# Performance work log

Measured on AMD Instinct MI355X. Metric: run time of the kernel, lower is better.

Reference implementation:

```python
import jax, jax.numpy as jnp
import numpy as np
import math

NHID = 32
FEAT_SIZE = 32
FEAT_SIZE_LIST = [16, 32, 32, 32]
SEQ_LEN = len(FEAT_SIZE_LIST)   # 4
N_EDGE_LABELS = 3
NLAYERS = 2
N_GRAPHS = 64
FINAL = SEQ_LEN * NHID          # 128


def _pos_enc(max_len, dim):
    pe = np.zeros((max_len, dim), dtype=np.float32)
    pos = np.arange(max_len, dtype=np.float32)[:, None]
    div = np.exp(np.arange(0, dim, 2, dtype=np.float32) * (-math.log(10000.0) / dim))
    pe[:, 0::2] = np.sin(pos * div)
    pe[:, 1::2] = np.cos(pos * div)
    return jnp.asarray(pe)


def _feature_attention(x, wqkv, w1, b1, w2, b2):
    # x: [N, S*NHID] -> attention over the S feature 'tokens' per node
    N, D = x.shape
    S = D // NHID
    xr = x.reshape(N, S, NHID)
    qkv = jnp.einsum('nsf,fh->nsh', xr, wqkv)          # [N,S,3*NHID]
    q, k, v = jnp.split(qkv, 3, axis=-1)
    att = jax.nn.softmax(jnp.einsum('nsh,nth->nst', q, k) / jnp.sqrt(jnp.asarray(NHID, x.dtype)), axis=-1)
    y = jnp.einsum('nst,nth->nsh', att, v)             # [N,S,NHID]
    y = y + (jax.nn.relu(y @ w1 + b1) @ w2 + b2)       # residual FFN
    return y.reshape(N, -1)


def setup_inputs() -> dict:
    key = jax.random.key(0)
    ks = jax.random.split(key, 16)
    N = 100000
    E = 800000
    inp = {
        'x': jax.random.normal(ks[0], (N, 112), dtype=jnp.float32),
        'edge_index0': jax.random.randint(ks[1], (2, E), 0, N),
        'edge_index1': jax.random.randint(ks[2], (2, E), 0, N),
        'edge_index2': jax.random.randint(ks[3], (2, E), 0, N),
        'batch': jnp.sort(jax.random.randint(ks[4], (N,), 0, N_GRAPHS)),
    }
    s = 0.05
    # FeatureLinear encoder (bias-free)
    inp['W_emb'] = jax.random.normal(ks[5], (FEAT_SIZE, NHID), dtype=jnp.float32) * s
    # Per layer: [root, conv0, conv1, conv2] FeatureAttention params, stacked
    A = 1 + N_EDGE_LABELS
    inp['qkv'] = jax.random.normal(ks[6], (NLAYERS, A, NHID, 3 * NHID), dtype=jnp.float32) * s
    inp['ffn_w1'] = jax.random.normal(ks[7], (NLAYERS, A, NHID, NHID), dtype=jnp.float32) * s
    inp['ffn_b1'] = jnp.zeros((NLAYERS, A, NHID), dtype=jnp.float32)
    inp['ffn_w2'] = jax.random.normal(ks[8], (NLAYERS, A, NHID, NHID), dtype=jnp.float32) * s
    inp['ffn_b2'] = jnp.zeros((NLAYERS, A, NHID), dtype=jnp.float32)
    # Heuristic decoder MLP: 128 -> 128 -> 1
    inp['mlp_w1'] = jax.random.normal(ks[9], (FINAL, FINAL), dtype=jnp.float32) * s
    inp['mlp_b1'] = jnp.zeros((FINAL,), dtype=jnp.float32)
    inp['mlp_w2'] = jax.random.normal(ks[10], (FINAL, 1), dtype=jnp.float32) * s
    inp['mlp_b2'] = jnp.zeros((1,), dtype=jnp.float32)
    return inp


def reference(x, edge_index0, edge_index1, edge_index2, batch,
              W_emb, qkv, ffn_w1, ffn_b1, ffn_w2, ffn_b2,
              mlp_w1, mlp_b1, mlp_w2, mlp_b2):
    N = x.shape[0]
    edge_indices = [edge_index0, edge_index1, edge_index2]

    # padding: split by feat_size_list, right-pad each chunk to FEAT_SIZE
    offs = np.cumsum(FEAT_SIZE_LIST)[:-1].tolist()
    chunks = jnp.split(x, offs, axis=1)
    padded = [jnp.pad(c, ((0, 0), (0, FEAT_SIZE - c.shape[1]))) for c in chunks]
    h = jnp.concatenate(padded, axis=1)                       # [N, SEQ_LEN*FEAT_SIZE]

    # sinusoidal positional encoding over the SEQ_LEN feature tokens
    pe = _pos_enc(10, FEAT_SIZE)[:SEQ_LEN]                    # [SEQ_LEN, FEAT_SIZE]
    h = (h.reshape(N, SEQ_LEN, FEAT_SIZE) + pe[None]).reshape(N, -1)

    # FeatureLinear encoder: per-token linear FEAT_SIZE -> NHID
    h = jnp.einsum('nsf,fh->nsh', h.reshape(N, SEQ_LEN, FEAT_SIZE), W_emb).reshape(N, -1)

    # RGNN layers: root attention + per-edge-label attention->scatter-sum
    for l in range(NLAYERS):
        x_out = _feature_attention(h, qkv[l, 0], ffn_w1[l, 0], ffn_b1[l, 0], ffn_w2[l, 0], ffn_b2[l, 0])
        for e in range(N_EDGE_LABELS):
            a = e + 1
            xt = _feature_attention(h, qkv[l, a], ffn_w1[l, a], ffn_b1[l, a], ffn_w2[l, a], ffn_b2[l, a])
            src, dst = edge_indices[e][0], edge_indices[e][1]
            x_out = x_out + jax.ops.segment_sum(xt[src], dst, num_segments=N)
        h = jax.nn.relu(x_out)

    # global mean pool over graphs
    sums = jax.ops.segment_sum(h, batch, num_segments=N_GRAPHS)
    cnts = jax.ops.segment_sum(jnp.ones((N,), h.dtype), batch, num_segments=N_GRAPHS)
    g = sums / jnp.maximum(cnts, 1.0)[:, None]                # [G, FINAL]

    # heuristic decoder
    out = jax.nn.relu(g @ mlp_w1 + mlp_b1) @ mlp_w2 + mlp_b2  # [G, 1]
    return out.squeeze(1)                                     # [G]
```

## Files before the change

### kernel.cpp

```cpp
#include <hip/hip_runtime.h>
#include <hip/hip_bf16.h>
#include <cstdint>
#include <cstddef>


typedef __attribute__((ext_vector_type(8))) short bf16x8;
typedef __attribute__((ext_vector_type(4))) float f32x4;
typedef __attribute__((ext_vector_type(2))) float f32x2;

#if defined(__has_builtin)
#if __has_builtin(__builtin_amdgcn_cvt_pk_fp8_f32) && __has_builtin(__builtin_amdgcn_cvt_pk_f32_fp8)
#define HW_FP8 1
#endif
#if __has_builtin(__builtin_amdgcn_cvt_pk_bf16_f32)
#define HW_PKBF16 1
#endif
#endif

__device__ inline short f2bf(float f) {
    union { float f; unsigned u; } v; v.f = f;
    unsigned r = (v.u + 0x7FFFu + ((v.u >> 16) & 1u)) >> 16;
    return (short)r;
}
__device__ inline float bf2f(unsigned short b) {
    union { unsigned u; float f; } v; v.u = ((unsigned)b) << 16;
    return v.f;
}
#ifdef HW_PKBF16
typedef __attribute__((ext_vector_type(2))) __bf16 bf16x2_t;
__device__ inline unsigned pk2(float a, float b) {
    union { bf16x2_t v; unsigned u; } c;
    c.v = __builtin_amdgcn_cvt_pk_bf16_f32(a, b);
    return c.u;
}
#else
__device__ inline unsigned pk2(float a, float b) {
    unsigned ua = __float_as_uint(a) + 0x8000u;
    unsigned ub = __float_as_uint(b) + 0x8000u;
    return __builtin_amdgcn_perm(ub, ua, 0x07060302u);
}
#endif

#ifndef HW_FP8
__device__ inline unsigned char f2fp8_sw(float f) {
    unsigned s = (__float_as_uint(f) >> 31) & 1u;
    float a = fminf(fabsf(f), 448.f);
    unsigned char bits;
    if (a < 0.015625f) {
        bits = (unsigned char)__float2int_rn(a * 512.f);
    } else {
        int e; float m = frexpf(a, &e);
        int mf = __float2int_rn(m * 16.f);
        if (mf == 16) { mf = 8; e += 1; }
        int ef = e - 1 + 7;
        if (ef > 15) { ef = 15; mf = 14; }
        bits = (unsigned char)((ef << 3) | (mf & 7));
    }
    return (unsigned char)((s << 7) | bits);
}
__device__ inline float fp82f_sw(unsigned b) {
    int s = (b >> 7) & 1, e = (b >> 3) & 15, m = b & 7;
    float v = e ? ldexpf((float)(8 + m), e - 10) : ldexpf((float)m, -9);
    return s ? -v : v;
}
#endif

__device__ inline unsigned pk4fp8(float v0, float v1, float v2, float v3) {
#ifdef HW_FP8
    int w = __builtin_amdgcn_cvt_pk_fp8_f32(v0, v1, 0, false);
    w = __builtin_amdgcn_cvt_pk_fp8_f32(v2, v3, w, true);
    return (unsigned)w;
#else
    return (unsigned)f2fp8_sw(v0) | ((unsigned)f2fp8_sw(v1) << 8) |
           ((unsigned)f2fp8_sw(v2) << 16) | ((unsigned)f2fp8_sw(v3) << 24);
#endif
}
__device__ inline float2 up2fp8(unsigned short raw) {
#ifdef HW_FP8
    f32x2 f = __builtin_amdgcn_cvt_pk_f32_fp8((int)(unsigned)raw, false);
    return make_float2(f[0], f[1]);
#else
    return make_float2(fp82f_sw(raw & 0xffu), fp82f_sw((raw >> 8) & 0xffu));
#endif
}

__device__ inline void acc8(float* a, uint2 v) {
#ifdef HW_FP8
    f32x2 f0 = __builtin_amdgcn_cvt_pk_f32_fp8((int)v.x, false);
    f32x2 f1 = __builtin_amdgcn_cvt_pk_f32_fp8((int)v.x, true);
    f32x2 f2 = __builtin_amdgcn_cvt_pk_f32_fp8((int)v.y, false);
    f32x2 f3 = __builtin_amdgcn_cvt_pk_f32_fp8((int)v.y, true);
    a[0] += f0[0]; a[1] += f0[1]; a[2] += f1[0]; a[3] += f1[1];
    a[4] += f2[0]; a[5] += f2[1]; a[6] += f3[0]; a[7] += f3[1];
#else
    unsigned b0 = v.x, b1 = v.y;
#pragma unroll
    for (int j = 0; j < 4; ++j) a[j]     += fp82f_sw((b0 >> (8 * j)) & 0xffu);
#pragma unroll
    for (int j = 0; j < 4; ++j) a[4 + j] += fp82f_sw((b1 >> (8 * j)) & 0xffu);
#endif
}

__global__ __launch_bounds__(64) void wprep_kernel(
    const float* __restrict__ qkv, const float* __restrict__ fw1,
    const float* __restrict__ fw2, unsigned short* __restrict__ wpack,
    int* __restrict__ bcnt, int* __restrict__ gres,
    float* __restrict__ gsum, float* __restrict__ gcnt)
{
    const int pi = blockIdx.x;
    const int lane = threadIdx.x;
    const int gid = pi * 64 + lane;
    for (int i = gid; i < 256; i += 512) { bcnt[i] = 0; gres[i] = 0; }
    for (int i = gid; i < 64 * 128; i += 512) gsum[i] = 0.f;
    if (gid < 64) gcnt[gid] = 0.f;

    const int q = lane >> 4, m = lane & 15;
    const float* Wq = qkv + (size_t)pi * 32 * 96;
    const float* W1 = fw1 + (size_t)pi * 32 * 32;
    const float* W2 = fw2 + (size_t)pi * 32 * 32;
    unsigned short* dst = wpack + (size_t)pi * 10 * 64 * 8;
#pragma unroll
    for (int ci = 0; ci < 6; ++ci)
#pragma unroll
        for (int j = 0; j < 8; ++j)
            dst[(ci * 64 + lane) * 8 + j] =
                (unsigned short)f2bf(Wq[(q * 8 + j) * 96 + ci * 16 + m]);
#pragma unroll
    for (int t = 0; t < 2; ++t)
#pragma unroll
        for (int j = 0; j < 8; ++j) {
            dst[((6 + t) * 64 + lane) * 8 + j] =
                (unsigned short)f2bf(W1[(q * 8 + j) * 32 + t * 16 + m]);
            dst[((8 + t) * 64 + lane) * 8 + j] =
                (unsigned short)f2bf(W2[(q * 8 + j) * 32 + t * 16 + m]);
        }
}

__global__ __launch_bounds__(128) void enc_kernel(
    const float* __restrict__ x, const float* __restrict__ Wemb,
    unsigned short* __restrict__ h, int N)
{
    __shared__ float sxr[8 * 112];
    __shared__ float spe[128];
    __shared__ float sW[1024];
    const int t = threadIdx.x;
    const int n0 = blockIdx.x * 8;

    {
        int s = t >> 5, f = t & 31;
        int i2 = f >> 1;
        float div = __expf(-(float)(2 * i2) * (logf(10000.0f) / 32.0f));
        float ang = (float)s * div;
        spe[t] = (f & 1) ? cosf(ang) : sinf(ang);
    }
    for (int i = t; i < 1024; i += 128) sW[i] = Wemb[i];
    for (int i = t; i < 8 * 112; i += 128) {
        int n = n0 + i / 112;
        sxr[i] = (n < N) ? x[(size_t)n0 * 112 + i] : 0.f;
    }
    __syncthreads();

    const int ts = t >> 5, c = t & 31;
    const int offs_[4] = {0, 16, 48, 80};
    const int lens_[4] = {16, 32, 32, 32};
    const int off = offs_[ts], len = lens_[ts];

    float acc[8];
#pragma unroll
    for (int i = 0; i < 8; ++i) acc[i] = 0.f;
    float pw = 0.f;
    for (int f = 0; f < 32; ++f) {
        float wv = sW[f * 32 + c];
        float pv = spe[ts * 32 + f];
        pw += pv * wv;
        if (f < len) {
#pragma unroll
            for (int i = 0; i < 8; ++i) acc[i] += sxr[i * 112 + off + f] * wv;
        }
    }
#pragma unroll
    for (int i = 0; i < 8; ++i) {
        int n = n0 + i;
        if (n < N)
            h[(size_t)n * 128 + ts * 32 + c] = (unsigned short)f2bf(acc[i] + pw);
    }
}

#define ATT_WAVES 4
#define WLDS 5376

__global__ __launch_bounds__(256, 3) void attn4_kernel(
    const unsigned short* __restrict__ in,
    unsigned short* __restrict__ outR, unsigned char* __restrict__ out3,
    const unsigned short* __restrict__ wpack,
    const float* __restrict__ fb1, const float* __restrict__ fb2,
    int pibase, int N)
{
    __shared__ char smem[ATT_WAVES * 2 * WLDS];
    const int lane = threadIdx.x & 63;
    const int wave = threadIdx.x >> 6;
    const int q = lane >> 4;
    const int m = lane & 15;

    char* wb0 = smem + wave * (2 * WLDS);

#pragma unroll
    for (int u = 0; u < 2; ++u) {
        int* p32 = (int*)(wb0 + u * WLDS + 4096);
        for (int i = lane; i < 320; i += 64) p32[i] = 0;
    }

    const f32x4 zf = {0.f, 0.f, 0.f, 0.f};
    const int pi = pibase + wave;
    unsigned char* out8 = out3 + (size_t)(wave - 1) * N * 128;

    bf16x8 wqkv[6], w1f[2], w2f[2];
    float b1r[2][4], b2r[2][4];
    {
        const unsigned short* wp = wpack + ((size_t)pi * 10 * 64 + lane) * 8;
#pragma unroll
        for (int ci = 0; ci < 6; ++ci)
            wqkv[ci] = *(const bf16x8*)(wp + ci * 64 * 8);
#pragma unroll
        for (int t = 0; t < 2; ++t) {
            w1f[t] = *(const bf16x8*)(wp + (6 + t) * 64 * 8);
            w2f[t] = *(const bf16x8*)(wp + (8 + t) * 64 * 8);
#pragma unroll
            for (int r = 0; r < 4; ++r) {
                b1r[t][r] = fb1[pi * 32 + 16 * t + q * 4 + r];
                b2r[t][r] = fb2[pi * 32 + 16 * t + q * 4 + r];
            }
        }
    }

    const int nsuper = (N + 7) >> 3;
    for (int stile = blockIdx.x; stile < nsuper; stile += gridDim.x) {
        const int n0 = stile * 8;

        bf16x8 ax[2];
#pragma unroll
        for (int u = 0; u < 2; ++u) {
            bf16x8 a = {0, 0, 0, 0, 0, 0, 0, 0};
            int nm = n0 + 4 * u + (m >> 2);
            if (nm < N)
                a = *(const bf16x8*)(in + (size_t)(n0 + 4 * u) * 128 + m * 32 + q * 8);
            ax[u] = a;
        }

#pragma unroll
        for (int u = 0; u < 2; ++u) {
            char* wbu = wb0 + u * WLDS;
            short* Qb = (short*)(wbu);
            short* Kb = (short*)(wbu + 1280);
            short* VT = (short*)(wbu + 2560);
            short* Pb = (short*)(wbu + 4096);

            f32x4 aQ[2], aK[2], aV[2];
#pragma unroll
            for (int t = 0; t < 2; ++t) {
                aQ[t] = __builtin_amdgcn_mfma_f32_16x16x32_bf16(wqkv[t],     ax[u], zf, 0, 0, 0);
                aK[t] = __builtin_amdgcn_mfma_f32_16x16x32_bf16(wqkv[2 + t], ax[u], zf, 0, 0, 0);
                aV[t] = __builtin_amdgcn_mfma_f32_16x16x32_bf16(ax[u], wqkv[4 + t], zf, 0, 0, 0);
            }
#pragma unroll
            for (int t = 0; t < 2; ++t) {
                uint2 dq, dk, dv;
                dq.x = pk2(aQ[t][0], aQ[t][1]); dq.y = pk2(aQ[t][2], aQ[t][3]);
                dk.x = pk2(aK[t][0], aK[t][1]); dk.y = pk2(aK[t][2], aK[t][3]);
                dv.x = pk2(aV[t][0], aV[t][1]); dv.y = pk2(aV[t][2], aV[t][3]);
                *(uint2*)(Qb + m * 40 + 16 * t + q * 4) = dq;
                *(uint2*)(Kb + m * 40 + 16 * t + q * 4) = dk;
                *(uint2*)(VT + (16 * t + m) * 24 + q * 4) = dv;
            }

            bf16x8 aKf = *(const bf16x8*)(Kb + m * 40 + q * 8);
            bf16x8 bQf = *(const bf16x8*)(Qb + m * 40 + q * 8);
            f32x4 st = __builtin_amdgcn_mfma_f32_16x16x32_bf16(aKf, bQf, zf, 0, 0, 0);

            float v0 = st[0] * 0.1767766952966369f;
            float v1 = st[1] * 0.1767766952966369f;
            float v2 = st[2] * 0.1767766952966369f;
            float v3 = st[3] * 0.1767766952966369f;
            float mx = fmaxf(fmaxf(v0, v1), fmaxf(v2, v3));
            float e0 = __expf(v0 - mx), e1 = __expf(v1 - mx);
            float e2 = __expf(v2 - mx), e3 = __expf(v3 - mx);
            float inv = 1.0f / (e0 + e1 + e2 + e3);
            if (q == (m >> 2)) {
                uint2 dp;
                dp.x = pk2(e0 * inv, e1 * inv);
                dp.y = pk2(e2 * inv, e3 * inv);
                *(uint2*)(Pb + m * 40 + q * 4) = dp;
            }

            f32x4 y[2];
#pragma unroll
            for (int t = 0; t < 2; ++t) {
                bf16x8 aVf = {0, 0, 0, 0, 0, 0, 0, 0};
                bf16x8 bPf = {0, 0, 0, 0, 0, 0, 0, 0};
                if (q < 2) {
                    aVf = *(const bf16x8*)(VT + (16 * t + m) * 24 + q * 8);
                    bPf = *(const bf16x8*)(Pb + m * 40 + q * 8);
                }
                y[t] = __builtin_amdgcn_mfma_f32_16x16x32_bf16(aVf, bPf, zf, 0, 0, 0);
            }
#pragma unroll
            for (int t = 0; t < 2; ++t) {
                uint2 dy;
                dy.x = pk2(y[t][0], y[t][1]); dy.y = pk2(y[t][2], y[t][3]);
                *(uint2*)(Qb + m * 40 + 16 * t + q * 4) = dy;
            }

            bf16x8 bY = *(const bf16x8*)(Qb + m * 40 + q * 8);
            f32x4 z1[2];
#pragma unroll
            for (int t = 0; t < 2; ++t)
                z1[t] = __builtin_amdgcn_mfma_f32_16x16x32_bf16(w1f[t], bY, zf, 0, 0, 0);
#pragma unroll
            for (int t = 0; t < 2; ++t) {
                uint2 dz;
                dz.x = pk2(fmaxf(z1[t][0] + b1r[t][0], 0.f),
                           fmaxf(z1[t][1] + b1r[t][1], 0.f));
                dz.y = pk2(fmaxf(z1[t][2] + b1r[t][2], 0.f),
                           fmaxf(z1[t][3] + b1r[t][3], 0.f));
                *(uint2*)(Kb + m * 40 + 16 * t + q * 4) = dz;
            }

            bf16x8 bZ = *(const bf16x8*)(Kb + m * 40 + q * 8);
            f32x4 o[2];
#pragma unroll
            for (int t = 0; t < 2; ++t)
                o[t] = __builtin_amdgcn_mfma_f32_16x16x32_bf16(w2f[t], bZ, zf, 0, 0, 0);

            if (n0 + 4 * u + (m >> 2) < N) {
                if (wave == 0) {
#pragma unroll
                    for (int t = 0; t < 2; ++t) {
                        uint2 dd;
                        dd.x = pk2(y[t][0] + o[t][0] + b2r[t][0],
                                   y[t][1] + o[t][1] + b2r[t][1]);
                        dd.y = pk2(y[t][2] + o[t][2] + b2r[t][2],
                                   y[t][3] + o[t][3] + b2r[t][3]);
                        *(uint2*)(outR + (size_t)(n0 + 4 * u) * 128 + m * 32 + 16 * t + q * 4) = dd;
                    }
                } else {
#pragma unroll
                    for (int t = 0; t < 2; ++t) {
                        unsigned pw8 = pk4fp8(
                            (y[t][0] + o[t][0] + b2r[t][0]) * 16.f,
                            (y[t][1] + o[t][1] + b2r[t][1]) * 16.f,
                            (y[t][2] + o[t][2] + b2r[t][2]) * 16.f,
                            (y[t][3] + o[t][3] + b2r[t][3]) * 16.f);
                        *(unsigned*)(out8 + (size_t)(n0 + 4 * u) * 128 + m * 32 + 16 * t + q * 4) = pw8;
                    }
                }
            }
        }
    }
}

#define PA_CHUNK 4096
#define PA_SHIFT 9
#define PA_MAXB  256
#define HB_K     16

__global__ __launch_bounds__(256) void histB_kernel(
    const int* __restrict__ e0, const int* __restrict__ e1,
    const int* __restrict__ e2, int* __restrict__ bcnt, int E)
{
    __shared__ int lh[PA_MAXB];
    const int lab = blockIdx.y;
    const int* e = (lab == 0) ? e0 : (lab == 1) ? e1 : e2;
    const int t = threadIdx.x;
    for (int i = t; i < PA_MAXB; i += 256) lh[i] = 0;
    __syncthreads();
    const int base = blockIdx.x * 256 * HB_K;
#pragma unroll
    for (int k = 0; k < HB_K; ++k) {
        int i = base + k * 256 + t;
        if (i < E) atomicAdd(&lh[e[E + i] >> PA_SHIFT], 1);
    }
    __syncthreads();
    for (int i = t; i < PA_MAXB; i += 256)
        if (lh[i]) atomicAdd(&bcnt[i], lh[i]);
}

__global__ __launch_bounds__(256) void bscan_kernel(
    const int* __restrict__ bcnt, int* __restrict__ bbase)
{
    __shared__ int sd[PA_MAXB];
    const int t = threadIdx.x;
    sd[t] = bcnt[t];
    __syncthreads();
    int own = sd[t];
    for (int o = 1; o < 256; o <<= 1) {
        int v = (t >= o) ? sd[t - o] : 0;
        __syncthreads();
        sd[t] += v;
        __syncthreads();
    }
    bbase[t] = sd[t] - own;
}

__global__ __launch_bounds__(256) void placeA_kernel(
    const int* __restrict__ e0, const int* __restrict__ e1, const int* __restrict__ e2,
    const int* __restrict__ bbase, int* __restrict__ gres,
    int2* __restrict__ pairs, int E, int N)
{
    __shared__ int2 sStage[PA_CHUNK];
    __shared__ int sCnt[PA_MAXB], sScan[PA_MAXB], sCur[PA_MAXB], sGB[PA_MAXB];

    const int lab = blockIdx.y;
    const int t = threadIdx.x;
    const int base = blockIdx.x * PA_CHUNK;
    const int* e = (lab == 0) ? e0 : (lab == 1) ? e1 : e2;
    const int srcoff = lab * N;
    const int nbins = (N + (1 << PA_SHIFT) - 1) >> PA_SHIFT;

    for (int i = t; i < PA_MAXB; i += 256) { sCnt[i] = 0; sCur[i] = 0; }
    __syncthreads();

    int msrc[16], mdst[16];
    const int cnt_total = min(PA_CHUNK, E - base);
#pragma unroll
    for (int k = 0; k < 16; ++k) {
        int i = base + k * 256 + t;
        if (i < E) {
            msrc[k] = srcoff + e[i];
            int d = e[E + i];
            mdst[k] = d;
            atomicAdd(&sCnt[d >> PA_SHIFT], 1);
        } else mdst[k] = -1;
    }
    __syncthreads();

    sScan[t] = sCnt[t];
    __syncthreads();
    for (int o = 1; o < 256; o <<= 1) {
        int v = (t >= o) ? sScan[t - o] : 0;
        __syncthreads();
        sScan[t] += v;
        __syncthreads();
    }
    if (t < nbins && sCnt[t] > 0)
        sGB[t] = bbase[t] + atomicAdd(&gres[t], sCnt[t]);
    __syncthreads();

#pragma unroll
    for (int k = 0; k < 16; ++k) {
        if (mdst[k] >= 0) {
            int bin = mdst[k] >> PA_SHIFT;
            int r = atomicAdd(&sCur[bin], 1);
            sStage[(sScan[bin] - sCnt[bin]) + r] = make_int2(msrc[k], mdst[k]);
        }
    }
    __syncthreads();

    for (int i = t; i < cnt_total; i += 256) {
        int2 pr = sStage[i];
        int bin = pr.y >> PA_SHIFT;
        pairs[sGB[bin] + (i - (sScan[bin] - sCnt[bin]))] = pr;
    }
}

__global__ __launch_bounds__(512) void placeB_kernel(
    const int2* __restrict__ pairs, const int* __restrict__ bbase,
    const int* __restrict__ bcnt, int* __restrict__ offs,
    int* __restrict__ csr, int N, int nbins)
{
    __shared__ int sCnt[512], sScan[512], sFill[512];
    const int bin = blockIdx.x;
    const int t = threadIdx.x;
    const int n0 = bin << PA_SHIFT;
    const int n1 = min(n0 + 512, N);
    const int len = n1 - n0;
    const int rb  = bbase[bin];
    const int cnt = bcnt[bin];
    const int2* gp = pairs + rb;

    sCnt[t] = 0; sFill[t] = 0;
    __syncthreads();
    for (int i = t; i < cnt; i += 512)
        atomicAdd(&sCnt[gp[i].y - n0], 1);
    __syncthreads();
    sScan[t] = sCnt[t];
    __syncthreads();
    for (int o = 1; o < 512; o <<= 1) {
        int v = (t >= o) ? sScan[t - o] : 0;
        __syncthreads();
        sScan[t] += v;
        __syncthreads();
    }
    const int excl = sScan[t] - sCnt[t];
    if (t < len) offs[n0 + t] = rb + excl;
    if (bin == nbins - 1 && t == 0) offs[N] = rb + cnt;
    sScan[t] = excl;
    __syncthreads();

    for (int i = t; i < cnt; i += 512) {
        int2 pr = gp[i];
        int ln = pr.y - n0;
        int p = atomicAdd(&sFill[ln], 1);
        csr[rb + sScan[ln] + p] = pr.x;
    }
}

__global__ __launch_bounds__(256) void agg3_kernel(
    const unsigned short* __restrict__ xtR,
    const unsigned char* __restrict__ xt3,
    const int* __restrict__ csr, const int* __restrict__ offs,
    unsigned short* __restrict__ hout, int N)
{
    const int w = threadIdx.x >> 6, lane = threadIdx.x & 63;
    const int dst = blockIdx.x * 4 + w;
    if (dst >= N) return;

    const int g = lane >> 4;
    const unsigned fl8 = (unsigned)(lane & 15) << 3;

    bf16x8 rv = *(const bf16x8*)(xtR + (size_t)dst * 128 + fl8);

    float a[8];
#pragma unroll
    for (int i = 0; i < 8; ++i) a[i] = 0.f;

    const int beg = offs[dst], end = offs[dst + 1];
    if (beg < end) {
        const int last = end - 1;
        int e0 = beg + g, e1 = beg + 4 + g;
        int c0 = csr[min(e0, last)];
        int c1 = csr[min(e1, last)];
        c0 = (e0 > last) ? -1 : c0;
        c1 = (e1 > last) ? -1 : c1;
        for (int k = beg; k < end; k += 8) {
            const int nk = k + 8;
            unsigned s0 = (unsigned)max(c0, 0);
            unsigned s1 = (unsigned)max(c1, 0);
            uint2 v0 = *(const uint2*)(xt3 + (s0 << 7) + fl8);
            uint2 v1 = *(const uint2*)(xt3 + (s1 << 7) + fl8);
            int ne0 = nk + g, ne1 = nk + 4 + g;
            int n0_ = csr[min(ne0, last)];
            int n1_ = csr[min(ne1, last)];
            n0_ = (ne0 > last) ? -1 : n0_;
            n1_ = (ne1 > last) ? -1 : n1_;
            v0.x = (c0 < 0) ? 0u : v0.x;  v0.y = (c0 < 0) ? 0u : v0.y;
            v1.x = (c1 < 0) ? 0u : v1.x;  v1.y = (c1 < 0) ? 0u : v1.y;
            acc8(a, v0);
            acc8(a, v1);
            c0 = n0_; c1 = n1_;
        }
    }

#pragma unroll
    for (int i = 0; i < 8; ++i) {
        a[i] += __shfl_xor(a[i], 16);
        a[i] += __shfl_xor(a[i], 32);
    }

    if (g == 0) {
        unsigned r[4];
#pragma unroll
        for (int t = 0; t < 4; ++t) {
            float f0 = bf2f((unsigned short)rv[2 * t])     + 0.0625f * a[2 * t];
            float f1 = bf2f((unsigned short)rv[2 * t + 1]) + 0.0625f * a[2 * t + 1];
            r[t] = pk2(fmaxf(f0, 0.f), fmaxf(f1, 0.f));
        }
        uint4 st = make_uint4(r[0], r[1], r[2], r[3]);
        *(uint4*)(hout + (size_t)dst * 128 + fl8) = st;
    }
}

__global__ __launch_bounds__(256) void pool_kernel(
    const unsigned short* __restrict__ in, const int* __restrict__ batch,
    float* __restrict__ gsum, float* __restrict__ gcnt, int N)
{
    int t = threadIdx.x;
    int j = t & 127, half = t >> 7;
    int n0 = blockIdx.x * 64 + half * 32;
    float acc = 0.f, c = 0.f; int cur = -1;
    for (int i = 0; i < 32; ++i) {
        int n = n0 + i;
        if (n >= N) break;
        int g = batch[n];
        if (g != cur) {
            if (cur >= 0) {
                atomicAdd(&gsum[cur * 128 + j], acc);
                if (j == 0) atomicAdd(&gcnt[cur], c);
            }
            cur = g; acc = 0.f; c = 0.f;
        }
        acc += bf2f(in[(size_t)n * 128 + j]);
        c += 1.f;
    }
    if (cur >= 0) {
        atomicAdd(&gsum[cur * 128 + j], acc);
        if (j == 0) atomicAdd(&gcnt[cur], c);
    }
}

__global__ __launch_bounds__(128) void dec_kernel(
    const float* __restrict__ gsum, const float* __restrict__ gcnt,
    const float* __restrict__ W1, const float* __restrict__ B1,
    const float* __restrict__ W2, const float* __restrict__ B2,
    float* __restrict__ out)
{
    __shared__ float sg[128];
    __shared__ float sh[128];
    int t = threadIdx.x, b = blockIdx.x;
    float cinv = 1.0f / fmaxf(gcnt[b], 1.0f);
    sg[t] = gsum[b * 128 + t] * cinv;
    __syncthreads();
    float acc = B1[t];
    for (int f = 0; f < 128; ++f) acc += sg[f] * W1[f * 128 + t];
    sh[t] = fmaxf(acc, 0.f) * W2[t];
    __syncthreads();
    for (int o = 64; o > 0; o >>= 1) {
        if (t < o) sh[t] += sh[t + o];
        __syncthreads();
    }
    if (t == 0) out[b] = sh[0] + B2[0];
}

extern "C" void kernel_launch(void* const* d_in, const int* in_sizes, int n_in,
                              void* d_out, int out_size, void* d_ws, size_t ws_size,
                              hipStream_t stream)
{
    const float* x    = (const float*)d_in[0];
    const int*   e0   = (const int*)d_in[1];
    const int*   e1   = (const int*)d_in[2];
    const int*   e2   = (const int*)d_in[3];
    const int*   bat  = (const int*)d_in[4];
    const float* Wemb = (const float*)d_in[5];
    const float* qkv  = (const float*)d_in[6];
    const float* fw1  = (const float*)d_in[7];
    const float* fb1  = (const float*)d_in[8];
    const float* fw2  = (const float*)d_in[9];
    const float* fb2  = (const float*)d_in[10];
    const float* mw1  = (const float*)d_in[11];
    const float* mb1  = (const float*)d_in[12];
    const float* mw2  = (const float*)d_in[13];
    const float* mb2  = (const float*)d_in[14];
    const int N = in_sizes[0] / 112;
    const int E = in_sizes[1] / 2;
    float* outp = (float*)d_out;
    (void)n_in; (void)out_size; (void)ws_size;

    char* w = (char*)d_ws;
    auto alloc = [&](size_t bytes) {
        char* p = w; w += (bytes + 255) & ~(size_t)255; return p;
    };
    unsigned short* h0    = (unsigned short*)alloc((size_t)N * 128 * 2);
    unsigned short* h1    = (unsigned short*)alloc((size_t)N * 128 * 2);
    unsigned short* xtR   = (unsigned short*)alloc((size_t)N * 128 * 2);
    unsigned char*  xt3   = (unsigned char*)alloc((size_t)3 * N * 128);
    unsigned short* wpack = (unsigned short*)alloc(8 * 10 * 64 * 8 * 2);
    int*   csr   = (int*)alloc((size_t)3 * E * 4);
    int*   offs  = (int*)alloc((size_t)(N + 1) * 4);
    int*   bcnt  = (int*)alloc(PA_MAXB * 4);
    int*   bbase = (int*)alloc(PA_MAXB * 4);
    int*   gres  = (int*)alloc(PA_MAXB * 4);
    float* gsum  = (float*)alloc(64 * 128 * 4);
    float* gcnt  = (float*)alloc(64 * 4);
    int2* pairs = (int2*)xtR;

    const int nbins = (N + (1 << PA_SHIFT) - 1) >> PA_SHIFT;

    wprep_kernel<<<8, 64, 0, stream>>>(qkv, fw1, fw2, wpack, bcnt, gres, gsum, gcnt);
    enc_kernel<<<(N + 7) / 8, 128, 0, stream>>>(x, Wemb, h0, N);

    histB_kernel<<<dim3((E + 256 * HB_K - 1) / (256 * HB_K), 3), 256, 0, stream>>>(
        e0, e1, e2, bcnt, E);
    bscan_kernel<<<1, 256, 0, stream>>>(bcnt, bbase);
    placeA_kernel<<<dim3((E + PA_CHUNK - 1) / PA_CHUNK, 3), 256, 0, stream>>>(
        e0, e1, e2, bbase, gres, pairs, E, N);
    placeB_kernel<<<nbins, 512, 0, stream>>>(pairs, bbase, bcnt, offs, csr, N, nbins);

    const int ATT_GRID = 768;
    auto run_layer = [&](const unsigned short* lin, unsigned short* lout, int l) {
        attn4_kernel<<<ATT_GRID, 256, 0, stream>>>(
            lin, xtR, xt3, wpack, fb1, fb2, l * 4, N);
        agg3_kernel<<<(N + 3) / 4, 256, 0, stream>>>(xtR, xt3, csr, offs, lout, N);
    };
    run_layer(h0, h1, 0);
    run_layer(h1, h0, 1);

    pool_kernel<<<(N + 63) / 64, 256, 0, stream>>>(h0, bat, gsum, gcnt, N);
    dec_kernel<<<64, 128, 0, stream>>>(gsum, gcnt, mw1, mb1, mw2, mb2, outp);
}
```

Before: 471.9 us.

## Restructure encoder: per-thread token outputs, precomputed positional bias, vectorized IO

The positional-encoding times W_emb term is now precomputed once inside the weight-prep kernel instead of in every encoder block. The encoder now handles 64 nodes per 256-thread block with float4 loads into padded LDS. Each thread computes all 32 outputs of one token, reading W_emb via uniform (scalar-cacheable) global loads, and writes packed bf16 with 16-byte stores. This cuts redundant sin/cos work, LDS traffic and narrow stores, at the cost of higher register use per thread.

```diff
diff --git a/kernel.cpp b/kernel.cpp
--- a/kernel.cpp
+++ b/kernel.cpp
@@ -103,7 +103,8 @@
 
 __global__ __launch_bounds__(64) void wprep_kernel(
     const float* __restrict__ qkv, const float* __restrict__ fw1,
-    const float* __restrict__ fw2, unsigned short* __restrict__ wpack,
+    const float* __restrict__ fw2, const float* __restrict__ Wemb,
+    unsigned short* __restrict__ wpack, float* __restrict__ pwc,
     int* __restrict__ bcnt, int* __restrict__ gres,
     float* __restrict__ gsum, float* __restrict__ gcnt)
 {
@@ -134,55 +135,85 @@
             dst[((8 + t) * 64 + lane) * 8 + j] =
                 (unsigned short)f2bf(W2[(q * 8 + j) * 32 + t * 16 + m]);
         }
-}
-
-__global__ __launch_bounds__(128) void enc_kernel(
+
+    if (pi == 0) {
+        const int c = lane & 31;
+        for (int ts = lane >> 5; ts < 4; ts += 2) {
+            float accp = 0.f;
+            for (int f = 0; f < 32; ++f) {
+                float div = __expf(-(float)(f & ~1) * (logf(10000.0f) / 32.0f));
+                float ang = (float)ts * div;
+                float pv = (f & 1) ? cosf(ang) : sinf(ang);
+                accp += pv * Wemb[f * 32 + c];
+            }
+            pwc[ts * 32 + c] = accp;
+        }
+    }
+}
+
+__global__ __launch_bounds__(256) void enc_kernel(
     const float* __restrict__ x, const float* __restrict__ Wemb,
-    unsigned short* __restrict__ h, int N)
-{
-    __shared__ float sxr[8 * 112];
-    __shared__ float spe[128];
-    __shared__ float sW[1024];
+    const float* __restrict__ pwc, unsigned short* __restrict__ h, int N)
+{
+    __shared__ float sx[64 * 116];
     const int t = threadIdx.x;
-    const int n0 = blockIdx.x * 8;
+    const int nbase = blockIdx.x * 64;
 
     {
-        int s = t >> 5, f = t & 31;
-        int i2 = f >> 1;
-        float div = __expf(-(float)(2 * i2) * (logf(10000.0f) / 32.0f));
-        float ang = (float)s * div;
-        spe[t] = (f & 1) ? cosf(ang) : sinf(ang);
-    }
-    for (int i = t; i < 1024; i += 128) sW[i] = Wemb[i];
-    for (int i = t; i < 8 * 112; i += 128) {
-        int n = n0 + i / 112;
-        sxr[i] = (n < N) ? x[(size_t)n0 * 112 + i] : 0.f;
-    }
-    __syncthreads();
-
-    const int ts = t >> 5, c = t & 31;
+        const float4* xg = (const float4*)x;
+        const size_t g4base = ((size_t)nbase * 112) >> 2;
+        const size_t lim4 = ((size_t)N * 112) >> 2;
+#pragma unroll
+        for (int rep = 0; rep < 7; ++rep) {
+            int i = t + rep * 256;
+            float4 v = make_float4(0.f, 0.f, 0.f, 0.f);
+            if (g4base + (size_t)i < lim4) v = xg[g4base + i];
+            int row = i / 28;
+            int col4 = i - row * 28;
+            *(float4*)&sx[row * 116 + col4 * 4] = v;
+        }
+    }
+    __syncthreads();
+
+    const int nl = t >> 2, ts = t & 3;
+    const int node = nbase + nl;
     const int offs_[4] = {0, 16, 48, 80};
-    const int lens_[4] = {16, 32, 32, 32};
-    const int off = offs_[ts], len = lens_[ts];
-
-    float acc[8];
-#pragma unroll
-    for (int i = 0; i < 8; ++i) acc[i] = 0.f;
-    float pw = 0.f;
+    const int nv_[4] = {4, 8, 8, 8};
+    const int off = offs_[ts];
+    const int nv = nv_[ts];
+
+    float xr[32];
+#pragma unroll
+    for (int j = 0; j < 8; ++j) {
+        float4 v = make_float4(0.f, 0.f, 0.f, 0.f);
+        if (j < nv) v = *(const float4*)&sx[nl * 116 + off + 4 * j];
+        *(float4*)&xr[4 * j] = v;
+    }
+
+    float acc[32];
+    {
+        const float4* pw4 = (const float4*)(pwc + ts * 32);
+#pragma unroll
+        for (int j = 0; j < 8; ++j) *(float4*)&acc[4 * j] = pw4[j];
+    }
+
+#pragma unroll
     for (int f = 0; f < 32; ++f) {
-        float wv = sW[f * 32 + c];
-        float pv = spe[ts * 32 + f];
-        pw += pv * wv;
-        if (f < len) {
-#pragma unroll
-            for (int i = 0; i < 8; ++i) acc[i] += sxr[i * 112 + off + f] * wv;
-        }
-    }
-#pragma unroll
-    for (int i = 0; i < 8; ++i) {
-        int n = n0 + i;
-        if (n < N)
-            h[(size_t)n * 128 + ts * 32 + c] = (unsigned short)f2bf(acc[i] + pw);
+        float xv = xr[f];
+#pragma unroll
+        for (int c = 0; c < 32; ++c)
+            acc[c] = fmaf(xv, Wemb[f * 32 + c], acc[c]);
+    }
+
+    if (node < N) {
+        unsigned rp[16];
+#pragma unroll
+        for (int j = 0; j < 16; ++j) rp[j] = pk2(acc[2 * j], acc[2 * j + 1]);
+        unsigned short* hp = h + (size_t)node * 128 + ts * 32;
+#pragma unroll
+        for (int j = 0; j < 4; ++j)
+            ((uint4*)hp)[j] = make_uint4(rp[4 * j], rp[4 * j + 1],
+                                         rp[4 * j + 2], rp[4 * j + 3]);
     }
 }
 
@@ -653,6 +684,7 @@
     unsigned short* xtR   = (unsigned short*)alloc((size_t)N * 128 * 2);
     unsigned char*  xt3   = (unsigned char*)alloc((size_t)3 * N * 128);
     unsigned short* wpack = (unsigned short*)alloc(8 * 10 * 64 * 8 * 2);
+    float* pwc   = (float*)alloc(128 * 4);
     int*   csr   = (int*)alloc((size_t)3 * E * 4);
     int*   offs  = (int*)alloc((size_t)(N + 1) * 4);
     int*   bcnt  = (int*)alloc(PA_MAXB * 4);
@@ -664,8 +696,9 @@
 
     const int nbins = (N + (1 << PA_SHIFT) - 1) >> PA_SHIFT;
 
-    wprep_kernel<<<8, 64, 0, stream>>>(qkv, fw1, fw2, wpack, bcnt, gres, gsum, gcnt);
-    enc_kernel<<<(N + 7) / 8, 128, 0, stream>>>(x, Wemb, h0, N);
+    wprep_kernel<<<8, 64, 0, stream>>>(qkv, fw1, fw2, Wemb, wpack, pwc,
+                                       bcnt, gres, gsum, gcnt);
+    enc_kernel<<<(N + 63) / 64, 256, 0, stream>>>(x, Wemb, pwc, h0, N);
 
     histB_kernel<<<dim3((E + 256 * HB_K - 1) / (256 * HB_K), 3), 256, 0, stream>>>(
         e0, e1, e2, bcnt, E);
```

Result: no change. 467.6 us (-0.9%).
